# Optimization experiments

Measured on AMD Instinct MI355X. Metric: run time of the kernel, lower is better.

## Reference

```python
import jax, jax.numpy as jnp
import numpy as np
import math

N, IN_DIM, Z, H, OUT, K = 16384, 64, 128, 1, 3, 16


def setup_inputs() -> dict:
    key = jax.random.key(0)
    ks = jax.random.split(key, 16)

    def lin(k, din, dout):
        kw, kb = jax.random.split(k)
        W = jax.random.normal(kw, (din, dout), jnp.float32) / math.sqrt(din)
        b = jax.random.normal(kb, (dout,), jnp.float32) * 0.01
        return W, b

    x = jax.random.normal(ks[0], (N, IN_DIM), jnp.float32)
    t = jnp.zeros((1,), jnp.float32)
    # layer dims: (in, heads*out) per TransformerConv
    dims = [(IN_DIM, Z * H), (Z * H, (Z // H) * H), (Z * H, (OUT // H) * H)]
    params = {}
    i = 1
    for li, (din, dout) in enumerate(dims, 1):
        for nm in ("q", "k", "v", "s"):
            W, b = lin(ks[i], din, dout)
            i += 1
            params[f"W{nm}{li}"] = W
            params[f"b{nm}{li}"] = b
    return {"t": t, "x": x, **params}


def knn_edge_index(coo, k):
    # kNN graph on 3-D coords (loop=False): edges neighbor(src) -> center(dst)
    n = coo.shape[0]
    sq = jnp.sum(coo * coo, axis=-1)
    d = sq[:, None] + sq[None, :] - 2.0 * (coo @ coo.T)  # [N, N] sq. distances
    d = d.at[jnp.arange(n), jnp.arange(n)].set(jnp.inf)  # exclude self-loops
    _, idx = jax.lax.top_k(-d, k)  # [N, K] nearest neighbor indices
    src = idx.reshape(-1)
    dst = jnp.repeat(jnp.arange(n), k)
    return src, dst


def tconv(x, src, dst, Wq, bq, Wk, bk, Wv, bv, Ws, bs, heads):
    # PyG TransformerConv (concat=True, root_weight=True, no edge_attr)
    n = x.shape[0]
    dout = Wq.shape[1]
    c = dout // heads
    q = (x @ Wq + bq).reshape(n, heads, c)
    kk = (x @ Wk + bk).reshape(n, heads, c)
    v = (x @ Wv + bv).reshape(n, heads, c)
    alpha = jnp.sum(q[dst] * kk[src], axis=-1) / math.sqrt(c)  # [E, H]
    amax = jax.ops.segment_max(alpha, dst, num_segments=n)
    ex = jnp.exp(alpha - amax[dst])
    denom = jax.ops.segment_sum(ex, dst, num_segments=n)
    w = ex / denom[dst]  # softmax over incoming edges per node
    msg = w[:, :, None] * v[src]  # [E, H, C]
    out = jax.ops.segment_sum(msg, dst, num_segments=n).reshape(n, dout)
    return out + x @ Ws + bs  # root/skip connection


def reference(t, x,
              Wq1, bq1, Wk1, bk1, Wv1, bv1, Ws1, bs1,
              Wq2, bq2, Wk2, bk2, Wv2, bv2, Ws2, bs2,
              Wq3, bq3, Wk3, bk3, Wv3, bv3, Ws3, bs3):
    src, dst = knn_edge_index(x[:, :3], K)  # built under no_grad in original
    h = jnp.tanh(tconv(x, src, dst, Wq1, bq1, Wk1, bk1, Wv1, bv1, Ws1, bs1, H))
    h = jnp.tanh(tconv(h, src, dst, Wq2, bq2, Wk2, bk2, Wv2, bv2, Ws2, bs2, H) + h)
    drift_coo = tconv(h, src, dst, Wq3, bq3, Wk3, bk3, Wv3, bv3, Ws3, bs3, H)
    return drift_coo
```

## Files before the change

### kernel.cpp

```cpp
#include <hip/hip_runtime.h>
#include <math.h>

#define NN 16384
#define QPW 2
#define CAP 128
#define WM 64
#define KTOP 17

typedef unsigned long long u64;

__global__ __launch_bounds__(256) void pack_coords(const float* __restrict__ x,
                                                   float4* __restrict__ coo) {
  int i = blockIdx.x * 256 + threadIdx.x;
  float a = x[i * 64 + 0];
  float b = x[i * 64 + 1];
  float c = x[i * 64 + 2];
  coo[i] = make_float4(a, b, c, a * a + b * b + c * c);
}

__device__ __forceinline__ int mbcnt64(u64 mask) {
  return __builtin_amdgcn_mbcnt_hi(
      (unsigned)(mask >> 32),
      __builtin_amdgcn_mbcnt_lo((unsigned)mask, 0));
}

__device__ __forceinline__ unsigned fmap(float d) {
  unsigned ub = __float_as_uint(d);
  return ub ^ ((unsigned)((int)ub >> 31) | 0x80000000u);
}

__device__ __forceinline__ float unfmap(unsigned ub) {
  unsigned fb = (ub & 0x80000000u) ? (ub ^ 0x80000000u) : ~ub;
  return __uint_as_float(fb);
}

__device__ __forceinline__ u64 u64min(u64 a, u64 b) { return a < b ? a : b; }
__device__ __forceinline__ u64 u64max(u64 a, u64 b) { return a > b ? a : b; }

__device__ __forceinline__ void sort128(u64& r0, u64& r1, int lane) {
#pragma unroll
  for (int k = 2; k <= 128; k <<= 1) {
    if (k == 128) {
      u64 lo = u64min(r0, r1);
      r1 = u64max(r0, r1);
      r0 = lo;
    }
#pragma unroll
    for (int jj = (k == 128 ? 32 : (k >> 1)); jj >= 1; jj >>= 1) {
      const bool up = (lane & jj) == 0;
      const bool asc0 = (lane & k) == 0;
      const bool asc1 = ((lane | 64) & k) == 0;
      u64 o0 = __shfl_xor(r0, jj);
      u64 o1 = __shfl_xor(r1, jj);
      r0 = (up == asc0) ? u64min(r0, o0) : u64max(r0, o0);
      r1 = (up == asc1) ? u64min(r1, o1) : u64max(r1, o1);
    }
  }
}

__device__ __forceinline__ void radix_shrink(u64* buf, int& cnt, float& th,
                                             int lane) {
  const u64 k0 = (lane < cnt) ? buf[lane] : ~0ull;
  const u64 k1 = (lane + 64 < cnt) ? buf[lane + 64] : ~0ull;
  const unsigned d0 = (unsigned)(k0 >> 32);
  const unsigned d1 = (unsigned)(k1 >> 32);
  unsigned p = 0u;
#pragma unroll
  for (int b = 31; b >= 0; --b) {
    const unsigned c = p | (1u << b);
    const u64 b0 = __ballot(d0 < c);
    const u64 b1 = __ballot(d1 < c);
    const int n = __popcll(b0) + __popcll(b1);
    if (n < KTOP) p = c;
  }
  const bool v0 = d0 <= p;
  const bool v1 = d1 <= p;
  const u64 m0 = __ballot(v0);
  const u64 m1 = __ballot(v1);
  const int base = __popcll(m0);
  if (v0) buf[mbcnt64(m0)] = k0;
  if (v1) buf[base + mbcnt64(m1)] = k1;
  cnt = base + __popcll(m1);
  th = unfmap(p);
}

__global__ __launch_bounds__(256) void knn_kernel(const float4* __restrict__ coo,
                                                  int* __restrict__ src) {
  __shared__ u64 bufs[4][QPW][CAP];
  const int lane = threadIdx.x & 63;
  const int wid = threadIdx.x >> 6;
  const int node0 = blockIdx.x * (4 * QPW) + wid * QPW;

  float nx[QPW], ny[QPW], nz[QPW], sq[QPW], th[QPW];
  int cnt[QPW];
#pragma unroll
  for (int q = 0; q < QPW; ++q) {
    const float4 me = coo[node0 + q];
    nx[q] = -2.0f * me.x;
    ny[q] = -2.0f * me.y;
    nz[q] = -2.0f * me.z;
    sq[q] = me.w;
    th[q] = __builtin_inff();
    cnt[q] = 0;
  }

  float4 ring[4];
#pragma unroll
  for (int u = 0; u < 4; ++u) ring[u] = coo[u * 64 + lane];

#pragma unroll 4
  for (int step = 0; step < NN / 64; ++step) {
    const int u = step & 3;
    const float4 cur = ring[u];
    if (step + 4 < NN / 64) ring[u] = coo[(step + 4) * 64 + lane];
    const int j = step * 64 + lane;

    float dd[QPW];
#pragma unroll
    for (int q = 0; q < QPW; ++q) {
      float a = fmaf(nz[q], cur.z, cur.w);
      a = fmaf(ny[q], cur.y, a);
      a = fmaf(nx[q], cur.x, a);
      dd[q] = sq[q] + a;
    }
    u64 mk[QPW];
#pragma unroll
    for (int q = 0; q < QPW; ++q) mk[q] = __ballot(dd[q] <= th[q]);

    if (mk[0] | mk[1]) {
#pragma unroll
      for (int q = 0; q < QPW; ++q) {
        if (mk[q]) {
          if (dd[q] <= th[q]) {
            const int pos = cnt[q] + mbcnt64(mk[q]);
            bufs[wid][q][pos] = ((u64)fmap(dd[q]) << 32) | (unsigned)j;
          }
          cnt[q] += __popcll(mk[q]);
        }
      }
      if ((cnt[0] >= WM) || (cnt[1] >= WM)) {
#pragma unroll
        for (int q = 0; q < QPW; ++q)
          if (cnt[q] >= WM) radix_shrink(bufs[wid][q], cnt[q], th[q], lane);
      }
    }
  }

#pragma unroll 1
  for (int q = 0; q < QPW; ++q) {
    u64 r0 = (lane < cnt[q]) ? bufs[wid][q][lane] : ~0ull;
    u64 r1 = (lane + 64 < cnt[q]) ? bufs[wid][q][lane + 64] : ~0ull;
    sort128(r0, r1, lane);
    const int idx = (int)(r0 & 0xFFFFFFFFull);
    const u64 selfm = __ballot((lane < KTOP) && (idx == node0 + q));
    const int s = selfm ? (__ffsll((long long)selfm) - 1) : 99;
    const int outrank = lane - (lane > s ? 1 : 0);
    if (lane < KTOP && lane != s && outrank < 16)
      src[(node0 + q) * 16 + outrank] = idx;
  }
}

template <int KD>
__global__ __launch_bounds__(256) void gemm_qkvs(
    const float* __restrict__ X, const float* __restrict__ W0,
    const float* __restrict__ W1, const float* __restrict__ W2,
    const float* __restrict__ W3, const float* __restrict__ B0,
    const float* __restrict__ B1, const float* __restrict__ B2,
    const float* __restrict__ B3, float* __restrict__ out) {
  __shared__ float As[64][68];
  __shared__ float Bs[64][64];
  const int brow = blockIdx.x * 64;
  const int by = blockIdx.y;
  const int wi = by >> 1;
  const float* W = wi == 0 ? W0 : wi == 1 ? W1 : wi == 2 ? W2 : W3;
  const float* bias = wi == 0 ? B0 : wi == 1 ? B1 : wi == 2 ? B2 : B3;
  const int cbase = (by & 1) * 64;
  const int tx = threadIdx.x & 15;
  const int ty = threadIdx.x >> 4;

  float acc[4][4] = {};
  for (int k0 = 0; k0 < KD; k0 += 64) {
    __syncthreads();
#pragma unroll
    for (int i = 0; i < 4; ++i) {
      const int flat = threadIdx.x * 4 + i * 1024;
      const int r = flat >> 6, kk = flat & 63;
      const float4 v = *(const float4*)&X[(brow + r) * KD + k0 + kk];
      As[kk + 0][r] = v.x;
      As[kk + 1][r] = v.y;
      As[kk + 2][r] = v.z;
      As[kk + 3][r] = v.w;
    }
#pragma unroll
    for (int i = 0; i < 4; ++i) {
      const int flat = threadIdx.x * 4 + i * 1024;
      const int kk = flat >> 6, c = flat & 63;
      *(float4*)&Bs[kk][c] = *(const float4*)&W[(k0 + kk) * 128 + cbase + c];
    }
    __syncthreads();
#pragma unroll 8
    for (int k = 0; k < 64; ++k) {
      const float4 a = *(const float4*)&As[k][ty * 4];
      const float4 b = *(const float4*)&Bs[k][tx * 4];
      const float av[4] = {a.x, a.y, a.z, a.w};
      const float bv[4] = {b.x, b.y, b.z, b.w};
#pragma unroll
      for (int i = 0; i < 4; ++i)
#pragma unroll
        for (int jj = 0; jj < 4; ++jj)
          acc[i][jj] = fmaf(av[i], bv[jj], acc[i][jj]);
    }
  }
  const float4 bi = *(const float4*)&bias[cbase + tx * 4];
#pragma unroll
  for (int i = 0; i < 4; ++i) {
    const int row = brow + ty * 4 + i;
    float4 o;
    o.x = acc[i][0] + bi.x;
    o.y = acc[i][1] + bi.y;
    o.z = acc[i][2] + bi.z;
    o.w = acc[i][3] + bi.w;
    *(float4*)&out[row * 512 + wi * 128 + cbase + tx * 4] = o;
  }
}

__global__ __launch_bounds__(256) void attn_c128(
    const float* __restrict__ qkvs, const int* __restrict__ src,
    const float* __restrict__ res, float* __restrict__ hout, int do_res) {
  const int lane = threadIdx.x & 63;
  const int node = blockIdx.x * 4 + (threadIdx.x >> 6);
  const float2 q2 = ((const float2*)(qkvs + node * 512))[lane];

  int nb[16];
#pragma unroll
  for (int r = 0; r < 16; ++r) nb[r] = src[node * 16 + r];

  float p[16];
#pragma unroll
  for (int r = 0; r < 16; ++r) {
    const float2 k2 = ((const float2*)(qkvs + nb[r] * 512 + 128))[lane];
    p[r] = q2.x * k2.x + q2.y * k2.y;
  }
#pragma unroll
  for (int o = 32; o; o >>= 1) {
#pragma unroll
    for (int r = 0; r < 16; ++r) p[r] += __shfl_xor(p[r], o);
  }

  float2 v2[16];
#pragma unroll
  for (int r = 0; r < 16; ++r)
    v2[r] = ((const float2*)(qkvs + nb[r] * 512 + 256))[lane];

  float m = p[0];
#pragma unroll
  for (int r = 1; r < 16; ++r) m = fmaxf(m, p[r]);
  float w[16];
  float den = 0.0f;
#pragma unroll
  for (int r = 0; r < 16; ++r) {
    w[r] = __expf((p[r] - m) * 0.088388347648318447f);
    den += w[r];
  }
  const float inv = 1.0f / den;
  float o0 = 0.0f, o1 = 0.0f;
#pragma unroll
  for (int r = 0; r < 16; ++r) {
    const float ww = w[r] * inv;
    o0 = fmaf(ww, v2[r].x, o0);
    o1 = fmaf(ww, v2[r].y, o1);
  }
  const float2 s2 = ((const float2*)(qkvs + node * 512 + 384))[lane];
  float r0 = o0 + s2.x;
  float r1 = o1 + s2.y;
  if (do_res) {
    const float2 h2 = ((const float2*)(res + node * 128))[lane];
    r0 += h2.x;
    r1 += h2.y;
  }
  ((float2*)(hout + node * 128))[lane] = make_float2(tanhf(r0), tanhf(r1));
}

__global__ __launch_bounds__(256) void gemm_qkvs3(
    const float* __restrict__ H, const float* __restrict__ W0,
    const float* __restrict__ W1, const float* __restrict__ W2,
    const float* __restrict__ W3, const float* __restrict__ B0,
    const float* __restrict__ B1, const float* __restrict__ B2,
    const float* __restrict__ B3, float* __restrict__ out) {
  __shared__ float hs[64][132];
  __shared__ float wsh[128 * 12];
  __shared__ float bsh[12];
  const int brow = blockIdx.x * 64;
  if (threadIdx.x < 12) {
    const int mi = threadIdx.x / 3, c = threadIdx.x % 3;
    const float* Bsel = mi == 0 ? B0 : mi == 1 ? B1 : mi == 2 ? B2 : B3;
    bsh[threadIdx.x] = Bsel[c];
  }
  for (int t = threadIdx.x; t < 1536; t += 256) {
    const int k = t / 12, cc = t % 12;
    const int mi = cc / 3, c = cc % 3;
    const float* Wsel = mi == 0 ? W0 : mi == 1 ? W1 : mi == 2 ? W2 : W3;
    wsh[t] = Wsel[k * 3 + c];
  }
#pragma unroll
  for (int i = 0; i < 8; ++i) {
    const int flat = threadIdx.x * 4 + i * 1024;
    const int r = flat >> 7, kk = flat & 127;
    *(float4*)&hs[r][kk] = *(const float4*)&H[(brow + r) * 128 + kk];
  }
  __syncthreads();
  const int r = threadIdx.x >> 2;
  const int part = threadIdx.x & 3;
  float a0 = 0.0f, a1 = 0.0f, a2 = 0.0f;
#pragma unroll 4
  for (int k = 0; k < 128; ++k) {
    const float h = hs[r][k];
    a0 = fmaf(h, wsh[k * 12 + part * 3 + 0], a0);
    a1 = fmaf(h, wsh[k * 12 + part * 3 + 1], a1);
    a2 = fmaf(h, wsh[k * 12 + part * 3 + 2], a2);
  }
  const int row = brow + r;
  out[row * 12 + part * 3 + 0] = a0 + bsh[part * 3 + 0];
  out[row * 12 + part * 3 + 1] = a1 + bsh[part * 3 + 1];
  out[row * 12 + part * 3 + 2] = a2 + bsh[part * 3 + 2];
}

__global__ __launch_bounds__(256) void attn_c3(const float* __restrict__ q3,
                                               const int* __restrict__ src,
                                               float* __restrict__ out) {
  const int gid = blockIdx.x * 256 + threadIdx.x;
  const int node = gid >> 4, r = gid & 15;
  const int j = src[node * 16 + r];
  const float* qn = q3 + node * 12;
  const float* kj = q3 + j * 12 + 3;
  float alpha = (qn[0] * kj[0] + qn[1] * kj[1] + qn[2] * kj[2]) *
                0.57735026918962576f;
  float m = alpha;
#pragma unroll
  for (int o = 8; o; o >>= 1) m = fmaxf(m, __shfl_xor(m, o, 16));
  const float e = __expf(alpha - m);
  float den = e;
#pragma unroll
  for (int o = 8; o; o >>= 1) den += __shfl_xor(den, o, 16);
  const float wgt = e / den;
  const float* vj = q3 + j * 12 + 6;
  float o0 = wgt * vj[0], o1 = wgt * vj[1], o2 = wgt * vj[2];
#pragma unroll
  for (int o = 8; o; o >>= 1) {
    o0 += __shfl_xor(o0, o, 16);
    o1 += __shfl_xor(o1, o, 16);
    o2 += __shfl_xor(o2, o, 16);
  }
  if (r == 0) {
    const float* sn = q3 + node * 12 + 9;
    out[node * 3 + 0] = o0 + sn[0];
    out[node * 3 + 1] = o1 + sn[1];
    out[node * 3 + 2] = o2 + sn[2];
  }
}

extern "C" void kernel_launch(void* const* d_in, const int* in_sizes, int n_in,
                              void* d_out, int out_size, void* d_ws,
                              size_t ws_size, hipStream_t stream) {
  const float* x = (const float*)d_in[1];
  const float* Wq1 = (const float*)d_in[2];
  const float* bq1 = (const float*)d_in[3];
  const float* Wk1 = (const float*)d_in[4];
  const float* bk1 = (const float*)d_in[5];
  const float* Wv1 = (const float*)d_in[6];
  const float* bv1 = (const float*)d_in[7];
  const float* Ws1 = (const float*)d_in[8];
  const float* bs1 = (const float*)d_in[9];
  const float* Wq2 = (const float*)d_in[10];
  const float* bq2 = (const float*)d_in[11];
  const float* Wk2 = (const float*)d_in[12];
  const float* bk2 = (const float*)d_in[13];
  const float* Wv2 = (const float*)d_in[14];
  const float* bv2 = (const float*)d_in[15];
  const float* Ws2 = (const float*)d_in[16];
  const float* bs2 = (const float*)d_in[17];
  const float* Wq3 = (const float*)d_in[18];
  const float* bq3 = (const float*)d_in[19];
  const float* Wk3 = (const float*)d_in[20];
  const float* bk3 = (const float*)d_in[21];
  const float* Wv3 = (const float*)d_in[22];
  const float* bv3 = (const float*)d_in[23];
  const float* Ws3 = (const float*)d_in[24];
  const float* bs3 = (const float*)d_in[25];

  char* ws = (char*)d_ws;
  float* qkvs = (float*)(ws);
  float* h1 = (float*)(ws + (size_t)32 * 1024 * 1024);
  float* h2 = (float*)(ws + (size_t)40 * 1024 * 1024);
  int* src = (int*)(ws + (size_t)48 * 1024 * 1024);
  float4* coo = (float4*)(ws + (size_t)49 * 1024 * 1024);
  float* q3 = (float*)(ws + (size_t)49 * 1024 * 1024 + 512 * 1024);
  float* out = (float*)d_out;

  pack_coords<<<NN / 256, 256, 0, stream>>>(x, coo);
  knn_kernel<<<NN / (4 * QPW), 256, 0, stream>>>(coo, src);
  gemm_qkvs<64><<<dim3(NN / 64, 8), 256, 0, stream>>>(
      x, Wq1, Wk1, Wv1, Ws1, bq1, bk1, bv1, bs1, qkvs);
  attn_c128<<<NN / 4, 256, 0, stream>>>(qkvs, src, nullptr, h1, 0);
  gemm_qkvs<128><<<dim3(NN / 64, 8), 256, 0, stream>>>(
      h1, Wq2, Wk2, Wv2, Ws2, bq2, bk2, bv2, bs2, qkvs);
  attn_c128<<<NN / 4, 256, 0, stream>>>(qkvs, src, h1, h2, 1);
  gemm_qkvs3<<<NN / 64, 256, 0, stream>>>(h2, Wq3, Wk3, Wv3, Ws3, bq3, bk3,
                                          bv3, bs3, q3);
  attn_c3<<<NN * 16 / 256, 256, 0, stream>>>(q3, src, out);
}
```

Measured before the change: 359.4 us.

## Seed kNN threshold from first candidates, process two tiles per step, widen attention loads

The kNN kernel now fills the buffer with the first 128 candidates and runs radix_shrink on them right away, so the threshold starts tight instead of at infinity. It then scans two 64-point tiles per loop step with a single combined ballot to skip tiles where no lane qualifies. The attention kernel maps 32 lanes per node with float4 loads instead of 64 lanes with float2, which halves the shuffle reduction depth and loads V inside the accumulate loop rather than buffering it. The aim is fewer early buffer fills and shrinks in kNN, fewer loop iterations, and more efficient gathers in attention, at the cost of extra branches and higher register pressure.

```diff
diff --git a/kernel.cpp b/kernel.cpp
--- a/kernel.cpp
+++ b/kernel.cpp
@@ -100,48 +100,73 @@
     ny[q] = -2.0f * me.y;
     nz[q] = -2.0f * me.z;
     sq[q] = me.w;
-    th[q] = __builtin_inff();
     cnt[q] = 0;
   }
 
-  float4 ring[4];
-#pragma unroll
-  for (int u = 0; u < 4; ++u) ring[u] = coo[u * 64 + lane];
-
-#pragma unroll 4
-  for (int step = 0; step < NN / 64; ++step) {
-    const int u = step & 3;
-    const float4 cur = ring[u];
-    if (step + 4 < NN / 64) ring[u] = coo[(step + 4) * 64 + lane];
-    const int j = step * 64 + lane;
-
-    float dd[QPW];
+  float4 ra[2], rb[2];
+  ra[0] = coo[lane];
+  rb[0] = coo[64 + lane];
+  ra[1] = coo[128 + lane];
+  rb[1] = coo[192 + lane];
+
+#pragma unroll
+  for (int q = 0; q < QPW; ++q) {
+    float d0 = sq[q] + fmaf(nx[q], ra[0].x,
+                            fmaf(ny[q], ra[0].y, fmaf(nz[q], ra[0].z, ra[0].w)));
+    float d1 = sq[q] + fmaf(nx[q], rb[0].x,
+                            fmaf(ny[q], rb[0].y, fmaf(nz[q], rb[0].z, rb[0].w)));
+    bufs[wid][q][lane] = ((u64)fmap(d0) << 32) | (unsigned)lane;
+    bufs[wid][q][64 + lane] = ((u64)fmap(d1) << 32) | (unsigned)(64 + lane);
+    cnt[q] = 128;
+    radix_shrink(bufs[wid][q], cnt[q], th[q], lane);
+  }
+
+  ra[0] = coo[256 + lane];
+  rb[0] = coo[256 + 64 + lane];
+
+#pragma unroll 2
+  for (int step = 1; step < NN / 128; ++step) {
+    const int u = step & 1;
+    const float4 c0 = ra[u];
+    const float4 c1 = rb[u];
+    if (step + 2 < NN / 128) {
+      ra[u] = coo[(step + 2) * 128 + lane];
+      rb[u] = coo[(step + 2) * 128 + 64 + lane];
+    }
+    const int j0 = step * 128 + lane;
+    const int j1 = j0 + 64;
+
+    float d0[QPW], d1[QPW];
+    bool a0[QPW], a1[QPW];
 #pragma unroll
     for (int q = 0; q < QPW; ++q) {
-      float a = fmaf(nz[q], cur.z, cur.w);
-      a = fmaf(ny[q], cur.y, a);
-      a = fmaf(nx[q], cur.x, a);
-      dd[q] = sq[q] + a;
-    }
-    u64 mk[QPW];
-#pragma unroll
-    for (int q = 0; q < QPW; ++q) mk[q] = __ballot(dd[q] <= th[q]);
-
-    if (mk[0] | mk[1]) {
+      d0[q] = sq[q] + fmaf(nx[q], c0.x,
+                           fmaf(ny[q], c0.y, fmaf(nz[q], c0.z, c0.w)));
+      d1[q] = sq[q] + fmaf(nx[q], c1.x,
+                           fmaf(ny[q], c1.y, fmaf(nz[q], c1.z, c1.w)));
+      a0[q] = d0[q] <= th[q];
+      a1[q] = d1[q] <= th[q];
+    }
+
+    if (__ballot(a0[0] | a1[0] | a0[1] | a1[1])) {
 #pragma unroll
       for (int q = 0; q < QPW; ++q) {
-        if (mk[q]) {
-          if (dd[q] <= th[q]) {
-            const int pos = cnt[q] + mbcnt64(mk[q]);
-            bufs[wid][q][pos] = ((u64)fmap(dd[q]) << 32) | (unsigned)j;
-          }
-          cnt[q] += __popcll(mk[q]);
+        const u64 m0 = __ballot(a0[q]);
+        if (m0) {
+          if (a0[q])
+            bufs[wid][q][cnt[q] + mbcnt64(m0)] =
+                ((u64)fmap(d0[q]) << 32) | (unsigned)j0;
+          cnt[q] += __popcll(m0);
+          if (cnt[q] >= WM) radix_shrink(bufs[wid][q], cnt[q], th[q], lane);
         }
-      }
-      if ((cnt[0] >= WM) || (cnt[1] >= WM)) {
-#pragma unroll
-        for (int q = 0; q < QPW; ++q)
+        const u64 m1 = __ballot(a1[q]);
+        if (m1) {
+          if (a1[q])
+            bufs[wid][q][cnt[q] + mbcnt64(m1)] =
+                ((u64)fmap(d1[q]) << 32) | (unsigned)j1;
+          cnt[q] += __popcll(m1);
           if (cnt[q] >= WM) radix_shrink(bufs[wid][q], cnt[q], th[q], lane);
+        }
       }
     }
   }
@@ -227,9 +252,10 @@
 __global__ __launch_bounds__(256) void attn_c128(
     const float* __restrict__ qkvs, const int* __restrict__ src,
     const float* __restrict__ res, float* __restrict__ hout, int do_res) {
-  const int lane = threadIdx.x & 63;
-  const int node = blockIdx.x * 4 + (threadIdx.x >> 6);
-  const float2 q2 = ((const float2*)(qkvs + node * 512))[lane];
+  const int g = threadIdx.x >> 5;
+  const int node = blockIdx.x * 8 + g;
+  const int c = threadIdx.x & 31;
+  const float4 q4 = ((const float4*)(qkvs + node * 512))[c];
 
   int nb[16];
 #pragma unroll
@@ -238,19 +264,14 @@
   float p[16];
 #pragma unroll
   for (int r = 0; r < 16; ++r) {
-    const float2 k2 = ((const float2*)(qkvs + nb[r] * 512 + 128))[lane];
-    p[r] = q2.x * k2.x + q2.y * k2.y;
-  }
-#pragma unroll
-  for (int o = 32; o; o >>= 1) {
+    const float4 k4 = ((const float4*)(qkvs + nb[r] * 512 + 128))[c];
+    p[r] = q4.x * k4.x + q4.y * k4.y + q4.z * k4.z + q4.w * k4.w;
+  }
+#pragma unroll
+  for (int o = 16; o; o >>= 1) {
 #pragma unroll
     for (int r = 0; r < 16; ++r) p[r] += __shfl_xor(p[r], o);
   }
-
-  float2 v2[16];
-#pragma unroll
-  for (int r = 0; r < 16; ++r)
-    v2[r] = ((const float2*)(qkvs + nb[r] * 512 + 256))[lane];
 
   float m = p[0];
 #pragma unroll
@@ -263,22 +284,27 @@
     den += w[r];
   }
   const float inv = 1.0f / den;
-  float o0 = 0.0f, o1 = 0.0f;
+  float o0 = 0.0f, o1 = 0.0f, o2 = 0.0f, o3 = 0.0f;
 #pragma unroll
   for (int r = 0; r < 16; ++r) {
+    const float4 v4 = ((const float4*)(qkvs + nb[r] * 512 + 256))[c];
     const float ww = w[r] * inv;
-    o0 = fmaf(ww, v2[r].x, o0);
-    o1 = fmaf(ww, v2[r].y, o1);
-  }
-  const float2 s2 = ((const float2*)(qkvs + node * 512 + 384))[lane];
-  float r0 = o0 + s2.x;
-  float r1 = o1 + s2.y;
+    o0 = fmaf(ww, v4.x, o0);
+    o1 = fmaf(ww, v4.y, o1);
+    o2 = fmaf(ww, v4.z, o2);
+    o3 = fmaf(ww, v4.w, o3);
+  }
+  const float4 s4 = ((const float4*)(qkvs + node * 512 + 384))[c];
+  float r0 = o0 + s4.x, r1 = o1 + s4.y, r2 = o2 + s4.z, r3 = o3 + s4.w;
   if (do_res) {
-    const float2 h2 = ((const float2*)(res + node * 128))[lane];
-    r0 += h2.x;
-    r1 += h2.y;
-  }
-  ((float2*)(hout + node * 128))[lane] = make_float2(tanhf(r0), tanhf(r1));
+    const float4 h4 = ((const float4*)(res + node * 128))[c];
+    r0 += h4.x;
+    r1 += h4.y;
+    r2 += h4.z;
+    r3 += h4.w;
+  }
+  ((float4*)(hout + node * 128))[c] =
+      make_float4(tanhf(r0), tanhf(r1), tanhf(r2), tanhf(r3));
 }
 
 __global__ __launch_bounds__(256) void gemm_qkvs3(
@@ -401,10 +427,10 @@
   knn_kernel<<<NN / (4 * QPW), 256, 0, stream>>>(coo, src);
   gemm_qkvs<64><<<dim3(NN / 64, 8), 256, 0, stream>>>(
       x, Wq1, Wk1, Wv1, Ws1, bq1, bk1, bv1, bs1, qkvs);
-  attn_c128<<<NN / 4, 256, 0, stream>>>(qkvs, src, nullptr, h1, 0);
+  attn_c128<<<NN / 8, 256, 0, stream>>>(qkvs, src, nullptr, h1, 0);
   gemm_qkvs<128><<<dim3(NN / 64, 8), 256, 0, stream>>>(
       h1, Wq2, Wk2, Wv2, Ws2, bq2, bk2, bv2, bs2, qkvs);
-  attn_c128<<<NN / 4, 256, 0, stream>>>(qkvs, src, h1, h2, 1);
+  attn_c128<<<NN / 8, 256, 0, stream>>>(qkvs, src, h1, h2, 1);
   gemm_qkvs3<<<NN / 64, 256, 0, stream>>>(h2, Wq3, Wk3, Wv3, Ws3, bq3, bk3,
                                           bv3, bs3, q3);
   attn_c3<<<NN * 16 / 256, 256, 0, stream>>>(q3, src, out);
```

Result: slower. 569.7 us (+58.5%).
